# Kernel optimization log

Measured on AMD Instinct MI355X. Metric: run time of the kernel, lower is better.

The kernel has to match this reference:

```python
import jax, jax.numpy as jnp
import numpy as np

JOINT_NUM = 25   # len(smpl_x.pos_joint_part['body'])
HM_D, HM_H, HM_W = 8, 8, 8
FEAT_DIM = 768


def setup_inputs() -> dict:
    key = jax.random.key(0)
    k1, k2, k3 = jax.random.split(key, 3)
    B = 512
    img_feat = jax.random.normal(k1, (B, FEAT_DIM, HM_H, HM_W), dtype=jnp.float32)
    out_ch = JOINT_NUM * HM_D  # 200
    # Conv2d 1x1 weight [out_ch, in_ch] and bias [out_ch]
    scale = 1.0 / np.sqrt(FEAT_DIM)
    conv_w = jax.random.uniform(k2, (out_ch, FEAT_DIM), jnp.float32, -scale, scale)
    conv_b = jax.random.uniform(k3, (out_ch,), jnp.float32, -scale, scale)
    return {"img_feat": img_feat, "conv_w": conv_w, "conv_b": conv_b}


def reference(img_feat, conv_w, conv_b):
    B = img_feat.shape[0]
    # 1x1 conv == per-pixel matmul over channels: bchw,oc -> bohw
    hm = jnp.einsum('bchw,oc->bohw', img_feat, conv_w) + conv_b[None, :, None, None]
    joint_hm_logits = hm.reshape(B, JOINT_NUM, HM_D, HM_H, HM_W)
    # softmax over flattened D*H*W
    flat = joint_hm_logits.reshape(B, JOINT_NUM, HM_D * HM_H * HM_W)
    p = jax.nn.softmax(flat, axis=2).reshape(B, JOINT_NUM, HM_D, HM_H, HM_W)
    # soft-argmax: marginal expectations along each axis
    accu_x = p.sum(axis=(2, 3))  # [B, J, W]
    accu_y = p.sum(axis=(2, 4))  # [B, J, H]
    accu_z = p.sum(axis=(3, 4))  # [B, J, D]
    x = (accu_x * jnp.arange(HM_W, dtype=jnp.float32)).sum(axis=2, keepdims=True)
    y = (accu_y * jnp.arange(HM_H, dtype=jnp.float32)).sum(axis=2, keepdims=True)
    z = (accu_z * jnp.arange(HM_D, dtype=jnp.float32)).sum(axis=2, keepdims=True)
    joint_coord = jnp.concatenate((x, y, z), axis=2)  # [B, J, 3]
    # original recomputes the same softmax for the returned heatmap
    joint_hm = p
    return (joint_hm, joint_coord)
```

## Files before the change

kernel.cpp:

```cpp
#include <hip/hip_runtime.h>


typedef __attribute__((ext_vector_type(4))) float f32x4;
typedef _Float16 f16x8 __attribute__((ext_vector_type(8)));
typedef unsigned short us8 __attribute__((ext_vector_type(8)));

namespace {
constexpr int kB = 512, kC = 768, kP = 64, kO = 200, kJ = 25;
constexpr int kSteps = 12;
constexpr int kNT = 13;
constexpr int kHR = 65;
constexpr int kWsFrag8 = 12 * 2 * 14 * 64;
constexpr size_t kHmOut = (size_t)kB * kJ * 512;
constexpr int kSmemBytes = kO * kHR * 4;
}

__global__ __launch_bounds__(256) void weight_half_kernel(
    const float* __restrict__ w, unsigned short* __restrict__ ws) {
  const int id = blockIdx.x * 256 + threadIdx.x;
  if (id >= kWsFrag8) return;
  const int ml = id & 15, g = (id >> 4) & 3;
  const int id2 = id >> 6;
  const int nt = id2 % 14;
  const int q = id2 / 14;
  const int n = nt * 16 + ml;
  const int kb = q * 32 + g * 8;
  union { _Float16 h[8]; us8 u; } pk;
#pragma unroll
  for (int i = 0; i < 8; ++i) {
    const float v = (n < kO) ? w[(size_t)n * kC + kb + i] : 0.f;
    pk.h[i] = (_Float16)v;
  }
  *(us8*)(ws + (size_t)id * 8) = pk.u;
}

__device__ inline int acell(int buf, int kc, int g, int px) {
  return (((buf * 2 + kc) * 4 + g) * 64 + px) * 8;
}

__global__ __launch_bounds__(512, 4) void posnet_fused_kernel(
    const float* __restrict__ img, const unsigned short* __restrict__ wsb,
    const float* __restrict__ bias, float* __restrict__ out) {
  __shared__ __align__(16) char smem[kSmemBytes];
  unsigned short* aLds = (unsigned short*)smem;
  float* hm = (float*)smem;

  const int b = blockIdx.x;
  const int tid = threadIdx.x;
  const int lane = tid & 63;
  const int wid = tid >> 6;
  const int ng = __builtin_amdgcn_readfirstlane(wid & 3);
  const int mh = __builtin_amdgcn_readfirstlane(wid >> 2);
  const int m_l = lane & 15;
  const int g = lane >> 4;
  const float* __restrict__ imgb = img + (size_t)b * kC * kP;

  const int sc0 = wid * 8;
  const int skc = sc0 >> 5;
  const int sg = (sc0 & 31) >> 3;

  f32x4 acc[4][2];
#pragma unroll
  for (int i = 0; i < 4; ++i)
#pragma unroll
    for (int j = 0; j < 2; ++j) acc[i][j] = f32x4{0.f, 0.f, 0.f, 0.f};

  float pf[8];
  auto load_pf = [&](int t) {
#pragma unroll
    for (int i = 0; i < 8; ++i)
      pf[i] = imgb[(size_t)(t * 64 + sc0 + i) * kP + lane];
  };
  auto cvt_write = [&](int buf) {
    union { _Float16 h[8]; us8 u; } pk;
#pragma unroll
    for (int i = 0; i < 8; ++i) pk.h[i] = (_Float16)pf[i];
    *(us8*)(aLds + acell(buf, skc, sg, lane)) = pk.u;
  };

  load_pf(0);
  cvt_write(0);
  __syncthreads();

  for (int t = 0; t < kSteps; ++t) {
    const int buf = t & 1;
    if (t + 1 < kSteps) load_pf(t + 1);
#pragma unroll
    for (int kc = 0; kc < 2; ++kc) {
      const f16x8 a0 = *(const f16x8*)(aLds + acell(buf, kc, g, mh * 32 + m_l));
      const f16x8 a1 =
          *(const f16x8*)(aLds + acell(buf, kc, g, mh * 32 + 16 + m_l));
#pragma unroll
      for (int ii = 0; ii < 4; ++ii) {
        const int nt = ii * 4 + ng;
        if (nt < kNT) {
          const f16x8 bb = *(const f16x8*)(
              wsb + ((size_t)(t * 2 + kc) * 14 + nt) * 512 + lane * 8);
          acc[ii][0] =
              __builtin_amdgcn_mfma_f32_16x16x32_f16(a0, bb, acc[ii][0], 0, 0, 0);
          acc[ii][1] =
              __builtin_amdgcn_mfma_f32_16x16x32_f16(a1, bb, acc[ii][1], 0, 0, 0);
        }
      }
    }
    if (t + 1 < kSteps) cvt_write((t + 1) & 1);
    __syncthreads();
  }

#pragma unroll
  for (int ii = 0; ii < 4; ++ii) {
    const int nt = ii * 4 + ng;
    if (nt < kNT) {
      const int o = nt * 16 + m_l;
      if (o < kO) {
        const float bo = bias[o];
#pragma unroll
        for (int mt = 0; mt < 2; ++mt) {
          const int m = (mh * 2 + mt) * 16 + g * 4;
#pragma unroll
          for (int r = 0; r < 4; ++r) hm[o * kHR + m + r] = acc[ii][mt][r] + bo;
        }
      }
    }
  }
  __syncthreads();

  for (int j = wid; j < kJ; j += 8) {
    float v[8];
#pragma unroll
    for (int k = 0; k < 8; ++k) v[k] = hm[(j * 8 + k) * kHR + lane];

    float m = v[0];
#pragma unroll
    for (int k = 1; k < 8; ++k) m = fmaxf(m, v[k]);
#pragma unroll
    for (int off = 32; off > 0; off >>= 1) m = fmaxf(m, __shfl_xor(m, off));

    float e[8];
    float s = 0.f;
#pragma unroll
    for (int k = 0; k < 8; ++k) {
      e[k] = __expf(v[k] - m);
      s += e[k];
    }
#pragma unroll
    for (int off = 32; off > 0; off >>= 1) s += __shfl_xor(s, off);
    const float inv = 1.0f / s;

    float psum = 0.f, zsum = 0.f;
    float* dst = out + ((size_t)b * kJ + j) * 512;
#pragma unroll
    for (int k = 0; k < 8; ++k) {
      const float pv = e[k] * inv;
      dst[k * 64 + lane] = pv;
      psum += pv;
      zsum += (float)k * pv;
    }
    float xs = (float)(lane & 7) * psum;
    float ys = (float)(lane >> 3) * psum;
#pragma unroll
    for (int off = 32; off > 0; off >>= 1) {
      xs += __shfl_xor(xs, off);
      ys += __shfl_xor(ys, off);
      zsum += __shfl_xor(zsum, off);
    }
    if (lane == 0) {
      float* cd = out + kHmOut + ((size_t)b * kJ + j) * 3;
      cd[0] = xs;
      cd[1] = ys;
      cd[2] = zsum;
    }
  }
}

extern "C" void kernel_launch(void* const* d_in, const int* in_sizes, int n_in,
                              void* d_out, int out_size, void* d_ws,
                              size_t ws_size, hipStream_t stream) {
  const float* img = (const float*)d_in[0];
  const float* w = (const float*)d_in[1];
  const float* bias = (const float*)d_in[2];
  unsigned short* wsb = (unsigned short*)d_ws;
  float* out = (float*)d_out;

  weight_half_kernel<<<dim3((kWsFrag8 + 255) / 256), dim3(256), 0, stream>>>(w, wsb);
  posnet_fused_kernel<<<dim3(kB), dim3(512), 0, stream>>>(img, wsb, bias, out);
}
```

Before: 170.7 us.

## Load A fragments directly from global memory, dropping LDS staging and barriers

Each wave now reads its image fragments straight from global memory, converts them to half in registers and feeds the MFMA. This removes the double-buffered LDS staging and the per-step __syncthreads. The price is that the four waves sharing a pixel half each load the same data, so caches see about four times the A traffic, with narrower 64-byte coalescing per row. The bias-add store into the heatmap tile becomes a 16-byte vector store, but the row stride of 65 floats means those stores are not 16-byte aligned.

```diff
diff --git a/kernel.cpp b/kernel.cpp
--- a/kernel.cpp
+++ b/kernel.cpp
@@ -12,7 +12,6 @@
 constexpr int kHR = 65;
 constexpr int kWsFrag8 = 12 * 2 * 14 * 64;
 constexpr size_t kHmOut = (size_t)kB * kJ * 512;
-constexpr int kSmemBytes = kO * kHR * 4;
 }
 
 __global__ __launch_bounds__(256) void weight_half_kernel(
@@ -34,16 +33,10 @@
   *(us8*)(ws + (size_t)id * 8) = pk.u;
 }
 
-__device__ inline int acell(int buf, int kc, int g, int px) {
-  return (((buf * 2 + kc) * 4 + g) * 64 + px) * 8;
-}
-
 __global__ __launch_bounds__(512, 4) void posnet_fused_kernel(
     const float* __restrict__ img, const unsigned short* __restrict__ wsb,
     const float* __restrict__ bias, float* __restrict__ out) {
-  __shared__ __align__(16) char smem[kSmemBytes];
-  unsigned short* aLds = (unsigned short*)smem;
-  float* hm = (float*)smem;
+  __shared__ __align__(16) float hm[kO * kHR];
 
   const int b = blockIdx.x;
   const int tid = threadIdx.x;
@@ -53,11 +46,9 @@
   const int mh = __builtin_amdgcn_readfirstlane(wid >> 2);
   const int m_l = lane & 15;
   const int g = lane >> 4;
-  const float* __restrict__ imgb = img + (size_t)b * kC * kP;
 
-  const int sc0 = wid * 8;
-  const int skc = sc0 >> 5;
-  const int sg = (sc0 & 31) >> 3;
+  const float* __restrict__ aBase =
+      img + (size_t)b * kC * kP + (size_t)(g * 8) * kP + mh * 32 + m_l;
 
   f32x4 acc[4][2];
 #pragma unroll
@@ -65,31 +56,22 @@
 #pragma unroll
     for (int j = 0; j < 2; ++j) acc[i][j] = f32x4{0.f, 0.f, 0.f, 0.f};
 
-  float pf[8];
-  auto load_pf = [&](int t) {
-#pragma unroll
-    for (int i = 0; i < 8; ++i)
-      pf[i] = imgb[(size_t)(t * 64 + sc0 + i) * kP + lane];
-  };
-  auto cvt_write = [&](int buf) {
-    union { _Float16 h[8]; us8 u; } pk;
-#pragma unroll
-    for (int i = 0; i < 8; ++i) pk.h[i] = (_Float16)pf[i];
-    *(us8*)(aLds + acell(buf, skc, sg, lane)) = pk.u;
-  };
-
-  load_pf(0);
-  cvt_write(0);
-  __syncthreads();
-
   for (int t = 0; t < kSteps; ++t) {
-    const int buf = t & 1;
-    if (t + 1 < kSteps) load_pf(t + 1);
 #pragma unroll
     for (int kc = 0; kc < 2; ++kc) {
-      const f16x8 a0 = *(const f16x8*)(aLds + acell(buf, kc, g, mh * 32 + m_l));
-      const f16x8 a1 =
-          *(const f16x8*)(aLds + acell(buf, kc, g, mh * 32 + 16 + m_l));
+      float a0f[8], a1f[8];
+      const float* ap = aBase + (size_t)(t * 64 + kc * 32) * kP;
+#pragma unroll
+      for (int e = 0; e < 8; ++e) {
+        a0f[e] = ap[(size_t)e * kP];
+        a1f[e] = ap[(size_t)e * kP + 16];
+      }
+      union { _Float16 h[8]; f16x8 v; } A0, A1;
+#pragma unroll
+      for (int e = 0; e < 8; ++e) {
+        A0.h[e] = (_Float16)a0f[e];
+        A1.h[e] = (_Float16)a1f[e];
+      }
 #pragma unroll
       for (int ii = 0; ii < 4; ++ii) {
         const int nt = ii * 4 + ng;
@@ -97,14 +79,12 @@
           const f16x8 bb = *(const f16x8*)(
               wsb + ((size_t)(t * 2 + kc) * 14 + nt) * 512 + lane * 8);
           acc[ii][0] =
-              __builtin_amdgcn_mfma_f32_16x16x32_f16(a0, bb, acc[ii][0], 0, 0, 0);
+              __builtin_amdgcn_mfma_f32_16x16x32_f16(A0.v, bb, acc[ii][0], 0, 0, 0);
           acc[ii][1] =
-              __builtin_amdgcn_mfma_f32_16x16x32_f16(a1, bb, acc[ii][1], 0, 0, 0);
+              __builtin_amdgcn_mfma_f32_16x16x32_f16(A1.v, bb, acc[ii][1], 0, 0, 0);
         }
       }
     }
-    if (t + 1 < kSteps) cvt_write((t + 1) & 1);
-    __syncthreads();
   }
 
 #pragma unroll
@@ -117,8 +97,10 @@
 #pragma unroll
         for (int mt = 0; mt < 2; ++mt) {
           const int m = (mh * 2 + mt) * 16 + g * 4;
+          f32x4 v;
 #pragma unroll
-          for (int r = 0; r < 4; ++r) hm[o * kHR + m + r] = acc[ii][mt][r] + bo;
+          for (int r = 0; r < 4; ++r) v[r] = acc[ii][mt][r] + bo;
+          *(f32x4*)(hm + o * kHR + m) = v;
         }
       }
     }
```

Measured after the change: 179.9 us. 1.05x slower.
